# Kernel optimization log

Hardware: AMD Instinct MI355X
Metric: run time of the kernel (lower is better)

Reference implementation:

```python
import jax, jax.numpy as jnp
import numpy as np

SEQ_LEN = 8192
D_K = 128
NEG_BIG = 1000000000.0


def setup_inputs() -> dict:
    key = jax.random.key(0)
    kq, kk, kv = jax.random.split(key, 3)
    q = jax.random.normal(kq, (SEQ_LEN, D_K), dtype=jnp.float32)
    k = jax.random.normal(kk, (SEQ_LEN, D_K), dtype=jnp.float32)
    v = jax.random.normal(kv, (SEQ_LEN, D_K), dtype=jnp.float32)
    return {"q": q, "k": k, "v": v}


def reference(q, k, v):
    # q,k,v: (S, d). Naive attention with causal (look-ahead) mask, masked=True.
    d_k = q.shape[-1]
    scaled_logits = jnp.matmul(q, k.T) / jnp.sqrt(jnp.asarray(d_k, q.dtype))  # (S, S)
    look_ahead_mask = jnp.triu(jnp.ones((SEQ_LEN, SEQ_LEN), dtype=q.dtype), k=1)
    scaled_logits = scaled_logits - look_ahead_mask * NEG_BIG
    attn = jnp.matmul(jax.nn.softmax(scaled_logits, axis=-1), v)  # (S, d)
    return attn
```

## Files before the change

### kernel.cpp

```cpp
#include <hip/hip_runtime.h>
#include <hip/hip_bf16.h>
#include <math.h>

#define S_LEN 8192
#define DK    128
#define BM    128
#define BN    64
#define NQT   (S_LEN / BM)
#define SCALE2 (0.08838834764831845f * 1.4426950408889634f)
#define DEFER_THR 5.0f

typedef __bf16 bf16x8_t __attribute__((ext_vector_type(8)));
typedef __bf16 bf16x4_t __attribute__((ext_vector_type(4)));
typedef __bf16 bf16x2_t __attribute__((ext_vector_type(2)));
typedef float  floatx16 __attribute__((ext_vector_type(16)));
typedef unsigned uintx4 __attribute__((ext_vector_type(4)));
typedef _Float16 half_t;
typedef _Float16 halfx4 __attribute__((ext_vector_type(4)));
typedef _Float16 halfx2 __attribute__((ext_vector_type(2)));

#define GLD16(g, l) __builtin_amdgcn_global_load_lds(                      \
    (const __attribute__((address_space(1))) void*)(g),                    \
    (__attribute__((address_space(3))) void*)(l), 16, 0, 0)

__device__ __forceinline__ float fexp2(float x) {
#if __has_builtin(__builtin_amdgcn_exp2f)
  return __builtin_amdgcn_exp2f(x);
#else
  return exp2f(x);
#endif
}

__device__ __forceinline__ unsigned pack2(float a, float b) {
  bf16x2_t w; w[0] = (__bf16)a; w[1] = (__bf16)b;
  return __builtin_bit_cast(unsigned, w);
}

__device__ __forceinline__ void xswap(unsigned &x, unsigned &y) {
#if __has_builtin(__builtin_amdgcn_permlane32_swap)
  typedef unsigned v2u __attribute__((ext_vector_type(2)));
  v2u t = __builtin_amdgcn_permlane32_swap(x, y, false, false);
  x = t[0]; y = t[1];
#else
  const unsigned sx = (unsigned)__shfl_xor((int)x, 32);
  const unsigned sy = (unsigned)__shfl_xor((int)y, 32);
  const bool lo = ((threadIdx.x & 63) < 32);
  const unsigned nx = lo ? x : sy;
  const unsigned ny = lo ? sx : y;
  x = nx; y = ny;
#endif
}

#define KBLOCKS ((S_LEN * DK) / (256 * 4))
__global__ __launch_bounds__(256) void prep_kv(const float* __restrict__ K,
                                               const float* __restrict__ V,
                                               __bf16* __restrict__ Kb,
                                               __bf16* __restrict__ Vt) {
  const int bx  = blockIdx.x;
  const int tid = threadIdx.x;
  if (bx < KBLOCKS) {
    const int i = (bx * 256 + tid) * 4;
    float4 v = *(const float4*)&K[i];
    bf16x4_t b;
    b[0] = (__bf16)v.x; b[1] = (__bf16)v.y; b[2] = (__bf16)v.z; b[3] = (__bf16)v.w;
    *(bf16x4_t*)&Kb[i] = b;
    return;
  }
  __shared__ __bf16 tl[64][34];
  const int vblk = bx - KBLOCKS;
  const int key0 = (vblk >> 2) * 64;
  const int d0   = (vblk & 3) * 32;
  {
    const int r = tid >> 2, fb = tid & 3;
    const float* vp = V + (size_t)(key0 + r) * DK + d0;
    #pragma unroll
    for (int h = 0; h < 2; ++h) {
      const int f = fb + h * 4;
      float4 v = *(const float4*)(vp + f * 4);
      tl[r][f * 4 + 0] = (__bf16)v.x; tl[r][f * 4 + 1] = (__bf16)v.y;
      tl[r][f * 4 + 2] = (__bf16)v.z; tl[r][f * 4 + 3] = (__bf16)v.w;
    }
  }
  __syncthreads();
  const int d = tid >> 3, kg = tid & 7;
  bf16x8_t b;
  #pragma unroll
  for (int j = 0; j < 8; ++j) b[j] = tl[kg * 8 + j][d];
  *(bf16x8_t*)&Vt[(size_t)(d0 + d) * S_LEN + key0 + kg * 8] = b;
}

__global__ __launch_bounds__(256, 2)
void fa_part(const float* __restrict__ Q, const __bf16* __restrict__ Kb,
             const __bf16* __restrict__ Vtg, float* __restrict__ Out,
             half_t* __restrict__ Opart, float* __restrict__ stats, int C) {
  __shared__ __align__(16) __bf16 Ks[2][BN * DK];
  __shared__ __align__(16) __bf16 Vts[DK * BN];

  const int tid  = threadIdx.x;
  const int wave = tid >> 6;
  const int lane = tid & 63;
  const int l31  = lane & 31;
  const int hh   = lane >> 5;

  const int qtile = (NQT - 1) - blockIdx.x;
  const int g     = blockIdx.y;
  const int nt    = 2 * qtile + 2;
  const int jb0   = g * C;
  if (jb0 >= nt) return;
  const int jb1 = (jb0 + C < nt) ? (jb0 + C) : nt;

  const int h2 = C >> 1;
  const int direct = (qtile < h2);
  const int ca = qtile / h2, cr = qtile - ca * h2;
  const int chunk = h2 * ca * (ca + 1) / 2 + cr * (ca + 1) - h2 + g;

  const int qw  = qtile * BM + wave * 32;
  const int myq = qw + l31;

  bf16x8_t qf[8];
  {
    const float* qrow = Q + (size_t)myq * DK + hh * 8;
    #pragma unroll
    for (int s = 0; s < 8; ++s) {
      float4 x = *(const float4*)(qrow + s * 16);
      float4 y = *(const float4*)(qrow + s * 16 + 4);
      bf16x8_t f;
      f[0]=(__bf16)(x.x*SCALE2); f[1]=(__bf16)(x.y*SCALE2);
      f[2]=(__bf16)(x.z*SCALE2); f[3]=(__bf16)(x.w*SCALE2);
      f[4]=(__bf16)(y.x*SCALE2); f[5]=(__bf16)(y.y*SCALE2);
      f[6]=(__bf16)(y.z*SCALE2); f[7]=(__bf16)(y.w*SCALE2);
      qf[s] = f;
    }
  }

  const __bf16* kp[4]; const __bf16* vp[4]; int loff[4];
  {
    const int ck = (lane & 15) ^ ((wave * 4 + (lane >> 4)) & 15);
    const int cv = (lane & 7) ^ ((lane >> 3) & 7);
    #pragma unroll
    for (int t = 0; t < 4; ++t) {
      const int rk = t * 16 + wave * 4 + (lane >> 4);
      kp[t] = Kb + ((size_t)(jb0 * BN + rk)) * DK + ck * 8;
      const int rv = t * 32 + wave * 8 + (lane >> 3);
      vp[t] = Vtg + (size_t)rv * S_LEN + jb0 * BN + cv * 8;
      loff[t] = t * 2048 + wave * 512;
    }
  }

  floatx16 o_acc[4];
  #pragma unroll
  for (int d = 0; d < 4; ++d)
    #pragma unroll
    for (int r = 0; r < 16; ++r) o_acc[d][r] = 0.f;
  float m_r = -INFINITY, l_r = 0.f;

  #pragma unroll
  for (int t = 0; t < 4; ++t) { GLD16(kp[t], &Ks[0][loff[t]]); kp[t] += BN * DK; }
  __syncthreads();

  int cur = 0;
  for (int jb = jb0; jb < jb1; ++jb) {
    #pragma unroll
    for (int t = 0; t < 4; ++t) { GLD16(vp[t], &Vts[loff[t]]); vp[t] += BN; }
    if (jb + 1 < jb1) {
      #pragma unroll
      for (int t = 0; t < 4; ++t) { GLD16(kp[t], &Ks[cur ^ 1][loff[t]]); kp[t] += BN * DK; }
    }

    const int active = (jb * 64 <= qw + 31);
    floatx16 sv[2];
    unsigned pk[4][4];

    if (active) {
      const __bf16* Kc = Ks[cur];

      bf16x8_t tf[16];
      #pragma unroll
      for (int g1 = 0; g1 < 2; ++g1) {
        const int row = g1 * 32 + l31;
        #pragma unroll
        for (int s = 0; s < 8; ++s)
          tf[g1 * 8 + s] = *(const bf16x8_t*)
              &Kc[row * DK + (((s * 2 + hh) ^ (row & 15)) * 8)];
      }
      __builtin_amdgcn_s_setprio(1);
      #pragma unroll
      for (int g1 = 0; g1 < 2; ++g1) {
        floatx16 acc;
        #pragma unroll
        for (int r = 0; r < 16; ++r) acc[r] = 0.f;
        #pragma unroll
        for (int s = 0; s < 8; ++s)
          acc = __builtin_amdgcn_mfma_f32_32x32x16_bf16(tf[g1 * 8 + s], qf[s],
                                                        acc, 0, 0, 0);
        sv[g1] = acc;
      }
      __builtin_amdgcn_s_setprio(0);

      if (jb * 64 + 63 > qw) {
        #pragma unroll
        for (int g1 = 0; g1 < 2; ++g1)
          #pragma unroll
          for (int r = 0; r < 16; ++r) {
            const int key = jb * 64 + g1 * 32 + (r & 3) + ((r >> 2) << 3) + (hh << 2);
            if (key > myq) sv[g1][r] = -1e30f;
          }
      }

      float pmx[4];
      #pragma unroll
      for (int i = 0; i < 4; ++i)
        pmx[i] = fmaxf(fmaxf(sv[0][i], sv[0][i + 4]),
                       fmaxf(sv[0][i + 8], sv[0][i + 12]));
      #pragma unroll
      for (int i = 0; i < 4; ++i)
        pmx[i] = fmaxf(pmx[i], fmaxf(fmaxf(sv[1][i], sv[1][i + 4]),
                                     fmaxf(sv[1][i + 8], sv[1][i + 12])));
      float pm = fmaxf(fmaxf(pmx[0], pmx[1]), fmaxf(pmx[2], pmx[3]));
      {
        unsigned b0 = __builtin_bit_cast(unsigned, pm), b1 = b0;
        xswap(b0, b1);
        pm = fmaxf(__builtin_bit_cast(float, b0), __builtin_bit_cast(float, b1));
      }

      if (__any(pm > m_r + DEFER_THR)) {
        const float mn = fmaxf(m_r, pm);
        const float al = fexp2(m_r - mn);
        m_r = mn; l_r *= al;
        #pragma unroll
        for (int d = 0; d < 4; ++d)
          #pragma unroll
          for (int r = 0; r < 16; ++r) o_acc[d][r] *= al;
      }

      float rsx[4] = {0.f, 0.f, 0.f, 0.f};
      #pragma unroll
      for (int g1 = 0; g1 < 2; ++g1)
        #pragma unroll
        for (int r = 0; r < 16; ++r) {
          const float pv = fexp2(sv[g1][r] - m_r);
          sv[g1][r] = pv;
          rsx[r & 3] += pv;
        }
      float rs = (rsx[0] + rsx[1]) + (rsx[2] + rsx[3]);
      {
        unsigned b0 = __builtin_bit_cast(unsigned, rs), b1 = b0;
        xswap(b0, b1);
        l_r += __builtin_bit_cast(float, b0) + __builtin_bit_cast(float, b1);
      }

      #pragma unroll
      for (int g1 = 0; g1 < 2; ++g1) {
        unsigned W0 = pack2(sv[g1][0],  sv[g1][1]);
        unsigned W1 = pack2(sv[g1][2],  sv[g1][3]);
        unsigned W2 = pack2(sv[g1][4],  sv[g1][5]);
        unsigned W3 = pack2(sv[g1][6],  sv[g1][7]);
        unsigned W4 = pack2(sv[g1][8],  sv[g1][9]);
        unsigned W5 = pack2(sv[g1][10], sv[g1][11]);
        unsigned W6 = pack2(sv[g1][12], sv[g1][13]);
        unsigned W7 = pack2(sv[g1][14], sv[g1][15]);
        xswap(W0, W2); xswap(W1, W3);
        xswap(W4, W6); xswap(W5, W7);
        pk[g1*2+0][0]=W0; pk[g1*2+0][1]=W1; pk[g1*2+0][2]=W2; pk[g1*2+0][3]=W3;
        pk[g1*2+1][0]=W4; pk[g1*2+1][1]=W5; pk[g1*2+1][2]=W6; pk[g1*2+1][3]=W7;
      }
    }

    __syncthreads();

    if (active) {
      bf16x8_t vf[16];
      #pragma unroll
      for (int ks = 0; ks < 4; ++ks)
        #pragma unroll
        for (int d = 0; d < 4; ++d) {
          const int row = d * 32 + l31;
          vf[ks * 4 + d] = *(const bf16x8_t*)
              &Vts[row * BN + (((ks * 2 + hh) ^ (row & 7)) * 8)];
        }
      __builtin_amdgcn_s_setprio(1);
      #pragma unroll
      for (int ks = 0; ks < 4; ++ks) {
        uintx4 u; u[0]=pk[ks][0]; u[1]=pk[ks][1]; u[2]=pk[ks][2]; u[3]=pk[ks][3];
        const bf16x8_t pf = __builtin_bit_cast(bf16x8_t, u);
        #pragma unroll
        for (int d = 0; d < 4; ++d)
          o_acc[d] = __builtin_amdgcn_mfma_f32_32x32x16_bf16(vf[ks * 4 + d], pf,
                                                             o_acc[d], 0, 0, 0);
      }
      __builtin_amdgcn_s_setprio(0);
    }

    __syncthreads();
    cur ^= 1;
  }

  if (direct) {
    const float inv = (l_r > 0.f) ? (1.0f / l_r) : 0.f;
    float* orow = Out + (size_t)myq * DK;
    #pragma unroll
    for (int d = 0; d < 4; ++d)
      #pragma unroll
      for (int mI = 0; mI < 4; ++mI) {
        float4 st;
        st.x = o_acc[d][mI*4+0] * inv; st.y = o_acc[d][mI*4+1] * inv;
        st.z = o_acc[d][mI*4+2] * inv; st.w = o_acc[d][mI*4+3] * inv;
        *(float4*)&orow[d * 32 + mI * 8 + hh * 4] = st;
      }
  } else {
    const float inv = (l_r > 0.f) ? (1.0f / l_r) : 0.f;
    half_t* orow = Opart + ((size_t)chunk * BM + wave * 32 + l31) * DK;
    #pragma unroll
    for (int d = 0; d < 4; ++d)
      #pragma unroll
      for (int mI = 0; mI < 4; ++mI) {
        halfx4 st;
        st[0] = (half_t)(o_acc[d][mI*4+0] * inv);
        st[1] = (half_t)(o_acc[d][mI*4+1] * inv);
        st[2] = (half_t)(o_acc[d][mI*4+2] * inv);
        st[3] = (half_t)(o_acc[d][mI*4+3] * inv);
        *(halfx4*)&orow[d * 32 + mI * 8 + hh * 4] = st;
      }
    if (hh == 0) {
      stats[((size_t)chunk * BM + wave * 32 + l31) * 2 + 0] = m_r;
      stats[((size_t)chunk * BM + wave * 32 + l31) * 2 + 1] = l_r;
    }
  }
}

__global__ __launch_bounds__(256)
void fa_reduce(const half_t* __restrict__ Opart, const float* __restrict__ stats,
               float* __restrict__ O, int C) {
  const int h2 = C >> 1;
  const int wave = threadIdx.x >> 6, lane = threadIdx.x & 63;
  const int row = h2 * BM + blockIdx.x * 4 + wave;
  const int qt = row >> 7, r = row & 127;

  const int a = qt / h2, rr = qt - a * h2;
  const int base = h2 * a * (a + 1) / 2 + rr * (a + 1) - h2;
  const int nch = (qt + h2) / h2;

  float M = -INFINITY;
  for (int g = 0; g < nch; ++g)
    M = fmaxf(M, stats[((size_t)(base + g) * BM + r) * 2]);

  float L = 0.f, ax = 0.f, ay = 0.f;
  for (int g = 0; g < nch; ++g) {
    const size_t sidx = (size_t)(base + g) * BM + r;
    const float m = stats[sidx * 2];
    const float wl = fexp2(m - M) * stats[sidx * 2 + 1];
    L += wl;
    halfx2 o = *(const halfx2*)&Opart[sidx * DK + lane * 2];
    ax += wl * (float)o[0]; ay += wl * (float)o[1];
  }
  const float inv = 1.f / L;
  float2 res; res.x = ax * inv; res.y = ay * inv;
  *(float2*)&O[(size_t)row * DK + lane * 2] = res;
}

extern "C" void kernel_launch(void* const* d_in, const int* in_sizes, int n_in,
                              void* d_out, int out_size, void* d_ws, size_t ws_size,
                              hipStream_t stream) {
  (void)in_sizes; (void)n_in; (void)out_size;
  const float* q = (const float*)d_in[0];
  const float* k = (const float*)d_in[1];
  const float* v = (const float*)d_in[2];
  float* out = (float*)d_out;

  const size_t conv_bytes = (size_t)S_LEN * DK * 2 * 2;
  const size_t per_chunk  = (size_t)BM * DK * 2 + 2 * BM * 4;

  int C = 2 * NQT; long long nc = 0;
  for (int c = 8; c < 2 * NQT; c += 2) {
    const int hh2 = c / 2;
    const int a = NQT / hh2, rr = NQT - a * hh2;
    const long long F64 = (long long)hh2 * a * (a + 1) / 2 + (long long)rr * (a + 1);
    const long long n = F64 - hh2;
    if (conv_bytes + (size_t)n * per_chunk <= ws_size) { C = c; nc = n; break; }
  }

  __bf16* Kb = (__bf16*)d_ws;
  __bf16* Vt = Kb + (size_t)S_LEN * DK;
  half_t* Opart = (half_t*)(Vt + (size_t)S_LEN * DK);
  float* stats = (float*)(Opart + (size_t)nc * BM * DK);

  prep_kv<<<KBLOCKS + 512, 256, 0, stream>>>(k, v, Kb, Vt);

  const int gy = (2 * NQT + C - 1) / C;
  fa_part<<<dim3(NQT, gy), 256, 0, stream>>>(q, Kb, Vt, out, Opart, stats, C);

  if (nc > 0) {
    const int h2 = C / 2;
    const int nrows = (NQT - h2) * BM;
    fa_reduce<<<nrows / 4, 256, 0, stream>>>(Opart, stats, out, C);
  }
}
```

Before: 124.9 us.

## Double-buffer V tiles and fuse split-K reduction into last-arriving block

```diff
diff --git a/kernel.cpp b/kernel.cpp
--- a/kernel.cpp
+++ b/kernel.cpp
@@ -9,6 +9,7 @@
 #define NQT   (S_LEN / BM)
 #define SCALE2 (0.08838834764831845f * 1.4426950408889634f)
 #define DEFER_THR 5.0f
+#define MAXCH 16
 
 typedef __bf16 bf16x8_t __attribute__((ext_vector_type(8)));
 typedef __bf16 bf16x4_t __attribute__((ext_vector_type(4)));
@@ -17,7 +18,6 @@
 typedef unsigned uintx4 __attribute__((ext_vector_type(4)));
 typedef _Float16 half_t;
 typedef _Float16 halfx4 __attribute__((ext_vector_type(4)));
-typedef _Float16 halfx2 __attribute__((ext_vector_type(2)));
 
 #define GLD16(g, l) __builtin_amdgcn_global_load_lds(                      \
     (const __attribute__((address_space(1))) void*)(g),                    \
@@ -55,9 +55,14 @@
 __global__ __launch_bounds__(256) void prep_kv(const float* __restrict__ K,
                                                const float* __restrict__ V,
                                                __bf16* __restrict__ Kb,
-                                               __bf16* __restrict__ Vt) {
+                                               __bf16* __restrict__ Vt,
+                                               unsigned* __restrict__ counters) {
   const int bx  = blockIdx.x;
   const int tid = threadIdx.x;
+  if (bx >= KBLOCKS + 512) {
+    if (tid < NQT) counters[tid] = 0u;
+    return;
+  }
   if (bx < KBLOCKS) {
     const int i = (bx * 256 + tid) * 4;
     float4 v = *(const float4*)&K[i];
@@ -92,9 +97,11 @@
 __global__ __launch_bounds__(256, 2)
 void fa_part(const float* __restrict__ Q, const __bf16* __restrict__ Kb,
              const __bf16* __restrict__ Vtg, float* __restrict__ Out,
-             half_t* __restrict__ Opart, float* __restrict__ stats, int C) {
+             half_t* __restrict__ Opart, float* __restrict__ stats,
+             unsigned* __restrict__ counters, int C) {
   __shared__ __align__(16) __bf16 Ks[2][BN * DK];
-  __shared__ __align__(16) __bf16 Vts[DK * BN];
+  __shared__ __align__(16) __bf16 Vts[2][DK * BN];
+  __shared__ int lastFlag;
 
   const int tid  = threadIdx.x;
   const int wave = tid >> 6;
@@ -112,7 +119,8 @@
   const int h2 = C >> 1;
   const int direct = (qtile < h2);
   const int ca = qtile / h2, cr = qtile - ca * h2;
-  const int chunk = h2 * ca * (ca + 1) / 2 + cr * (ca + 1) - h2 + g;
+  const int chunkBase = h2 * ca * (ca + 1) / 2 + cr * (ca + 1) - h2;
+  const int chunk = chunkBase + g;
 
   const int qw  = qtile * BM + wave * 32;
   const int myq = qw + l31;
@@ -155,44 +163,47 @@
   float m_r = -INFINITY, l_r = 0.f;
 
   #pragma unroll
-  for (int t = 0; t < 4; ++t) { GLD16(kp[t], &Ks[0][loff[t]]); kp[t] += BN * DK; }
-  __syncthreads();
+  for (int t = 0; t < 4; ++t) GLD16(kp[t], &Ks[0][loff[t]]);
+  #pragma unroll
+  for (int t = 0; t < 4; ++t) GLD16(vp[t], &Vts[0][loff[t]]);
+  if (jb0 + 1 < jb1) {
+    #pragma unroll
+    for (int t = 0; t < 4; ++t) { kp[t] += BN * DK; vp[t] += BN; }
+  }
 
   int cur = 0;
   for (int jb = jb0; jb < jb1; ++jb) {
     #pragma unroll
-    for (int t = 0; t < 4; ++t) { GLD16(vp[t], &Vts[loff[t]]); vp[t] += BN; }
-    if (jb + 1 < jb1) {
-      #pragma unroll
-      for (int t = 0; t < 4; ++t) { GLD16(kp[t], &Ks[cur ^ 1][loff[t]]); kp[t] += BN * DK; }
-    }
-
-    const int active = (jb * 64 <= qw + 31);
-    floatx16 sv[2];
-    unsigned pk[4][4];
-
-    if (active) {
+    for (int t = 0; t < 4; ++t) GLD16(kp[t], &Ks[cur ^ 1][loff[t]]);
+    #pragma unroll
+    for (int t = 0; t < 4; ++t) GLD16(vp[t], &Vts[cur ^ 1][loff[t]]);
+    if (jb + 2 < jb1) {
+      #pragma unroll
+      for (int t = 0; t < 4; ++t) { kp[t] += BN * DK; vp[t] += BN; }
+    }
+
+    asm volatile("s_waitcnt vmcnt(8)" ::: "memory");
+    __builtin_amdgcn_s_barrier();
+    __builtin_amdgcn_sched_barrier(0);
+
+    if (jb * 64 <= qw + 31) {
       const __bf16* Kc = Ks[cur];
-
-      bf16x8_t tf[16];
-      #pragma unroll
-      for (int g1 = 0; g1 < 2; ++g1) {
-        const int row = g1 * 32 + l31;
-        #pragma unroll
-        for (int s = 0; s < 8; ++s)
-          tf[g1 * 8 + s] = *(const bf16x8_t*)
-              &Kc[row * DK + (((s * 2 + hh) ^ (row & 15)) * 8)];
-      }
+      const __bf16* Vc = Vts[cur];
+
+      floatx16 sv[2];
       __builtin_amdgcn_s_setprio(1);
       #pragma unroll
       for (int g1 = 0; g1 < 2; ++g1) {
         floatx16 acc;
         #pragma unroll
         for (int r = 0; r < 16; ++r) acc[r] = 0.f;
-        #pragma unroll
-        for (int s = 0; s < 8; ++s)
-          acc = __builtin_amdgcn_mfma_f32_32x32x16_bf16(tf[g1 * 8 + s], qf[s],
-                                                        acc, 0, 0, 0);
+        const int row = g1 * 32 + l31;
+        #pragma unroll
+        for (int s = 0; s < 8; ++s) {
+          bf16x8_t kf = *(const bf16x8_t*)
+              &Kc[row * DK + (((s * 2 + hh) ^ (row & 15)) * 8)];
+          acc = __builtin_amdgcn_mfma_f32_32x32x16_bf16(kf, qf[s], acc, 0, 0, 0);
+        }
         sv[g1] = acc;
       }
       __builtin_amdgcn_s_setprio(0);
@@ -249,6 +260,7 @@
         l_r += __builtin_bit_cast(float, b0) + __builtin_bit_cast(float, b1);
       }
 
+      unsigned pk[4][4];
       #pragma unroll
       for (int g1 = 0; g1 < 2; ++g1) {
         unsigned W0 = pack2(sv[g1][0],  sv[g1][1]);
@@ -264,34 +276,25 @@
         pk[g1*2+0][0]=W0; pk[g1*2+0][1]=W1; pk[g1*2+0][2]=W2; pk[g1*2+0][3]=W3;
         pk[g1*2+1][0]=W4; pk[g1*2+1][1]=W5; pk[g1*2+1][2]=W6; pk[g1*2+1][3]=W7;
       }
-    }
-
-    __syncthreads();
-
-    if (active) {
-      bf16x8_t vf[16];
-      #pragma unroll
-      for (int ks = 0; ks < 4; ++ks)
-        #pragma unroll
-        for (int d = 0; d < 4; ++d) {
-          const int row = d * 32 + l31;
-          vf[ks * 4 + d] = *(const bf16x8_t*)
-              &Vts[row * BN + (((ks * 2 + hh) ^ (row & 7)) * 8)];
-        }
+
       __builtin_amdgcn_s_setprio(1);
       #pragma unroll
       for (int ks = 0; ks < 4; ++ks) {
         uintx4 u; u[0]=pk[ks][0]; u[1]=pk[ks][1]; u[2]=pk[ks][2]; u[3]=pk[ks][3];
         const bf16x8_t pf = __builtin_bit_cast(bf16x8_t, u);
         #pragma unroll
-        for (int d = 0; d < 4; ++d)
-          o_acc[d] = __builtin_amdgcn_mfma_f32_32x32x16_bf16(vf[ks * 4 + d], pf,
-                                                             o_acc[d], 0, 0, 0);
+        for (int d = 0; d < 4; ++d) {
+          const int row = d * 32 + l31;
+          bf16x8_t vf = *(const bf16x8_t*)
+              &Vc[row * BN + (((ks * 2 + hh) ^ (row & 7)) * 8)];
+          o_acc[d] = __builtin_amdgcn_mfma_f32_32x32x16_bf16(vf, pf, o_acc[d], 0, 0, 0);
+        }
       }
       __builtin_amdgcn_s_setprio(0);
     }
 
-    __syncthreads();
+    __builtin_amdgcn_s_barrier();
+    __builtin_amdgcn_sched_barrier(0);
     cur ^= 1;
   }
 
@@ -307,7 +310,10 @@
         st.z = o_acc[d][mI*4+2] * inv; st.w = o_acc[d][mI*4+3] * inv;
         *(float4*)&orow[d * 32 + mI * 8 + hh * 4] = st;
       }
-  } else {
+    return;
+  }
+
+  {
     const float inv = (l_r > 0.f) ? (1.0f / l_r) : 0.f;
     half_t* orow = Opart + ((size_t)chunk * BM + wave * 32 + l31) * DK;
     #pragma unroll
@@ -326,36 +332,51 @@
       stats[((size_t)chunk * BM + wave * 32 + l31) * 2 + 1] = l_r;
     }
   }
-}
-
-__global__ __launch_bounds__(256)
-void fa_reduce(const half_t* __restrict__ Opart, const float* __restrict__ stats,
-               float* __restrict__ O, int C) {
-  const int h2 = C >> 1;
-  const int wave = threadIdx.x >> 6, lane = threadIdx.x & 63;
-  const int row = h2 * BM + blockIdx.x * 4 + wave;
-  const int qt = row >> 7, r = row & 127;
-
-  const int a = qt / h2, rr = qt - a * h2;
-  const int base = h2 * a * (a + 1) / 2 + rr * (a + 1) - h2;
-  const int nch = (qt + h2) / h2;
-
-  float M = -INFINITY;
-  for (int g = 0; g < nch; ++g)
-    M = fmaxf(M, stats[((size_t)(base + g) * BM + r) * 2]);
-
-  float L = 0.f, ax = 0.f, ay = 0.f;
-  for (int g = 0; g < nch; ++g) {
-    const size_t sidx = (size_t)(base + g) * BM + r;
-    const float m = stats[sidx * 2];
-    const float wl = fexp2(m - M) * stats[sidx * 2 + 1];
-    L += wl;
-    halfx2 o = *(const halfx2*)&Opart[sidx * DK + lane * 2];
-    ax += wl * (float)o[0]; ay += wl * (float)o[1];
-  }
-  const float inv = 1.f / L;
-  float2 res; res.x = ax * inv; res.y = ay * inv;
-  *(float2*)&O[(size_t)row * DK + lane * 2] = res;
+
+  const int nch = (qtile + h2) / h2;
+  __threadfence();
+  __syncthreads();
+  if (tid == 0) {
+    const unsigned old = atomicAdd(&counters[qtile], 1u);
+    lastFlag = (old == (unsigned)(nch - 1)) ? 1 : 0;
+  }
+  __syncthreads();
+  if (!lastFlag) return;
+  __threadfence();
+
+  float* wlf = (float*)Ks;
+  if (tid < BM) {
+    const int r = tid;
+    float M = -INFINITY;
+    for (int g2 = 0; g2 < nch; ++g2)
+      M = fmaxf(M, stats[((size_t)(chunkBase + g2) * BM + r) * 2]);
+    float L = 0.f;
+    for (int g2 = 0; g2 < nch; ++g2) {
+      const size_t sidx = (size_t)(chunkBase + g2) * BM + r;
+      const float wv = fexp2(stats[sidx * 2] - M) * stats[sidx * 2 + 1];
+      wlf[r * (MAXCH + 1) + g2] = wv;
+      L += wv;
+    }
+    const float invL = 1.f / L;
+    for (int g2 = 0; g2 < nch; ++g2) wlf[r * (MAXCH + 1) + g2] *= invL;
+  }
+  __syncthreads();
+
+  #pragma unroll 4
+  for (int i = 0; i < 16; ++i) {
+    const int slot = tid + i * 256;
+    const int r = slot >> 5, c4 = slot & 31;
+    float ax = 0.f, ay = 0.f, az = 0.f, aw = 0.f;
+    for (int g2 = 0; g2 < nch; ++g2) {
+      const float w = wlf[r * (MAXCH + 1) + g2];
+      halfx4 o = *(const halfx4*)
+          &Opart[((size_t)(chunkBase + g2) * BM + r) * DK + c4 * 4];
+      ax += w * (float)o[0]; ay += w * (float)o[1];
+      az += w * (float)o[2]; aw += w * (float)o[3];
+    }
+    float4 res; res.x = ax; res.y = ay; res.z = az; res.w = aw;
+    *(float4*)&Out[((size_t)(qtile * BM + r)) * DK + c4 * 4] = res;
+  }
 }
 
 extern "C" void kernel_launch(void* const* d_in, const int* in_sizes, int n_in,
@@ -376,22 +397,18 @@
     const int a = NQT / hh2, rr = NQT - a * hh2;
     const long long F64 = (long long)hh2 * a * (a + 1) / 2 + (long long)rr * (a + 1);
     const long long n = F64 - hh2;
-    if (conv_bytes + (size_t)n * per_chunk <= ws_size) { C = c; nc = n; break; }
+    if (conv_bytes + (size_t)n * per_chunk + NQT * 4 <= ws_size) { C = c; nc = n; break; }
   }
 
   __bf16* Kb = (__bf16*)d_ws;
   __bf16* Vt = Kb + (size_t)S_LEN * DK;
   half_t* Opart = (half_t*)(Vt + (size_t)S_LEN * DK);
   float* stats = (float*)(Opart + (size_t)nc * BM * DK);
-
-  prep_kv<<<KBLOCKS + 512, 256, 0, stream>>>(k, v, Kb, Vt);
+  unsigned* counters = (unsigned*)(stats + (size_t)nc * BM * 2);
+
+  prep_kv<<<KBLOCKS + 513, 256, 0, stream>>>(k, v, Kb, Vt, counters);
 
   const int gy = (2 * NQT + C - 1) / C;
-  fa_part<<<dim3(NQT, gy), 256, 0, stream>>>(q, Kb, Vt, out, Opart, stats, C);
-
-  if (nc > 0) {
-    const int h2 = C / 2;
-    const int nrows = (NQT - h2) * BM;
-    fa_reduce<<<nrows / 4, 256, 0, stream>>>(Opart, stats, out, C);
-  }
-}
+  fa_part<<<dim3(NQT, gy), 256, 0, stream>>>(q, Kb, Vt, out, Opart, stats,
+                                             counters, C);
+}
```

New measurement: 226.9 us. 81.7% more time.

## Load K and V tiles directly from global into registers, dropping LDS staging

Applied to the files above, without the earlier changes.

```diff
diff --git a/kernel.cpp b/kernel.cpp
--- a/kernel.cpp
+++ b/kernel.cpp
@@ -18,10 +18,6 @@
 typedef _Float16 half_t;
 typedef _Float16 halfx4 __attribute__((ext_vector_type(4)));
 typedef _Float16 halfx2 __attribute__((ext_vector_type(2)));
-
-#define GLD16(g, l) __builtin_amdgcn_global_load_lds(                      \
-    (const __attribute__((address_space(1))) void*)(g),                    \
-    (__attribute__((address_space(3))) void*)(l), 16, 0, 0)
 
 __device__ __forceinline__ float fexp2(float x) {
 #if __has_builtin(__builtin_amdgcn_exp2f)
@@ -89,13 +85,10 @@
   *(bf16x8_t*)&Vt[(size_t)(d0 + d) * S_LEN + key0 + kg * 8] = b;
 }
 
-__global__ __launch_bounds__(256, 2)
+__global__ __launch_bounds__(256, 3)
 void fa_part(const float* __restrict__ Q, const __bf16* __restrict__ Kb,
              const __bf16* __restrict__ Vtg, float* __restrict__ Out,
              half_t* __restrict__ Opart, float* __restrict__ stats, int C) {
-  __shared__ __align__(16) __bf16 Ks[2][BN * DK];
-  __shared__ __align__(16) __bf16 Vts[DK * BN];
-
   const int tid  = threadIdx.x;
   const int wave = tid >> 6;
   const int lane = tid & 63;
@@ -116,6 +109,9 @@
 
   const int qw  = qtile * BM + wave * 32;
   const int myq = qw + l31;
+
+  const int jbw1_ = qtile * 2 + (wave >> 1) + 1;
+  const int jbw1 = (jb1 < jbw1_) ? jb1 : jbw1_;
 
   bf16x8_t qf[8];
   {
@@ -133,19 +129,14 @@
     }
   }
 
-  const __bf16* kp[4]; const __bf16* vp[4]; int loff[4];
-  {
-    const int ck = (lane & 15) ^ ((wave * 4 + (lane >> 4)) & 15);
-    const int cv = (lane & 7) ^ ((lane >> 3) & 7);
-    #pragma unroll
-    for (int t = 0; t < 4; ++t) {
-      const int rk = t * 16 + wave * 4 + (lane >> 4);
-      kp[t] = Kb + ((size_t)(jb0 * BN + rk)) * DK + ck * 8;
-      const int rv = t * 32 + wave * 8 + (lane >> 3);
-      vp[t] = Vtg + (size_t)rv * S_LEN + jb0 * BN + cv * 8;
-      loff[t] = t * 2048 + wave * 512;
-    }
-  }
+  const __bf16* kp[2];
+  const __bf16* vp[4];
+  #pragma unroll
+  for (int g1 = 0; g1 < 2; ++g1)
+    kp[g1] = Kb + ((size_t)(jb0 * BN + g1 * 32 + l31)) * DK + hh * 8;
+  #pragma unroll
+  for (int d = 0; d < 4; ++d)
+    vp[d] = Vtg + (size_t)(d * 32 + l31) * S_LEN + jb0 * BN + hh * 8;
 
   floatx16 o_acc[4];
   #pragma unroll
@@ -154,145 +145,121 @@
     for (int r = 0; r < 16; ++r) o_acc[d][r] = 0.f;
   float m_r = -INFINITY, l_r = 0.f;
 
-  #pragma unroll
-  for (int t = 0; t < 4; ++t) { GLD16(kp[t], &Ks[0][loff[t]]); kp[t] += BN * DK; }
-  __syncthreads();
-
-  int cur = 0;
-  for (int jb = jb0; jb < jb1; ++jb) {
-    #pragma unroll
-    for (int t = 0; t < 4; ++t) { GLD16(vp[t], &Vts[loff[t]]); vp[t] += BN; }
-    if (jb + 1 < jb1) {
-      #pragma unroll
-      for (int t = 0; t < 4; ++t) { GLD16(kp[t], &Ks[cur ^ 1][loff[t]]); kp[t] += BN * DK; }
-    }
-
-    const int active = (jb * 64 <= qw + 31);
+  for (int jb = jb0; jb < jbw1; ++jb) {
+    bf16x8_t kf[16];
+    #pragma unroll
+    for (int g1 = 0; g1 < 2; ++g1)
+      #pragma unroll
+      for (int s = 0; s < 8; ++s)
+        kf[g1 * 8 + s] = *(const bf16x8_t*)(kp[g1] + s * 16);
+
     floatx16 sv[2];
-    unsigned pk[4][4];
-
-    if (active) {
-      const __bf16* Kc = Ks[cur];
-
-      bf16x8_t tf[16];
-      #pragma unroll
-      for (int g1 = 0; g1 < 2; ++g1) {
-        const int row = g1 * 32 + l31;
-        #pragma unroll
-        for (int s = 0; s < 8; ++s)
-          tf[g1 * 8 + s] = *(const bf16x8_t*)
-              &Kc[row * DK + (((s * 2 + hh) ^ (row & 15)) * 8)];
-      }
-      __builtin_amdgcn_s_setprio(1);
-      #pragma unroll
-      for (int g1 = 0; g1 < 2; ++g1) {
-        floatx16 acc;
-        #pragma unroll
-        for (int r = 0; r < 16; ++r) acc[r] = 0.f;
-        #pragma unroll
-        for (int s = 0; s < 8; ++s)
-          acc = __builtin_amdgcn_mfma_f32_32x32x16_bf16(tf[g1 * 8 + s], qf[s],
-                                                        acc, 0, 0, 0);
-        sv[g1] = acc;
-      }
-      __builtin_amdgcn_s_setprio(0);
-
-      if (jb * 64 + 63 > qw) {
-        #pragma unroll
-        for (int g1 = 0; g1 < 2; ++g1)
-          #pragma unroll
-          for (int r = 0; r < 16; ++r) {
-            const int key = jb * 64 + g1 * 32 + (r & 3) + ((r >> 2) << 3) + (hh << 2);
-            if (key > myq) sv[g1][r] = -1e30f;
-          }
-      }
-
-      float pmx[4];
-      #pragma unroll
-      for (int i = 0; i < 4; ++i)
-        pmx[i] = fmaxf(fmaxf(sv[0][i], sv[0][i + 4]),
-                       fmaxf(sv[0][i + 8], sv[0][i + 12]));
-      #pragma unroll
-      for (int i = 0; i < 4; ++i)
-        pmx[i] = fmaxf(pmx[i], fmaxf(fmaxf(sv[1][i], sv[1][i + 4]),
-                                     fmaxf(sv[1][i + 8], sv[1][i + 12])));
-      float pm = fmaxf(fmaxf(pmx[0], pmx[1]), fmaxf(pmx[2], pmx[3]));
-      {
-        unsigned b0 = __builtin_bit_cast(unsigned, pm), b1 = b0;
-        xswap(b0, b1);
-        pm = fmaxf(__builtin_bit_cast(float, b0), __builtin_bit_cast(float, b1));
-      }
-
-      if (__any(pm > m_r + DEFER_THR)) {
-        const float mn = fmaxf(m_r, pm);
-        const float al = fexp2(m_r - mn);
-        m_r = mn; l_r *= al;
-        #pragma unroll
-        for (int d = 0; d < 4; ++d)
-          #pragma unroll
-          for (int r = 0; r < 16; ++r) o_acc[d][r] *= al;
-      }
-
-      float rsx[4] = {0.f, 0.f, 0.f, 0.f};
+    __builtin_amdgcn_s_setprio(1);
+    #pragma unroll
+    for (int g1 = 0; g1 < 2; ++g1) {
+      floatx16 acc;
+      #pragma unroll
+      for (int r = 0; r < 16; ++r) acc[r] = 0.f;
+      #pragma unroll
+      for (int s = 0; s < 8; ++s)
+        acc = __builtin_amdgcn_mfma_f32_32x32x16_bf16(kf[g1 * 8 + s], qf[s],
+                                                      acc, 0, 0, 0);
+      sv[g1] = acc;
+    }
+    __builtin_amdgcn_s_setprio(0);
+
+    bf16x8_t vf[16];
+    #pragma unroll
+    for (int ks = 0; ks < 4; ++ks)
+      #pragma unroll
+      for (int d = 0; d < 4; ++d)
+        vf[ks * 4 + d] = *(const bf16x8_t*)(vp[d] + ks * 16);
+
+    if (jb * 64 + 63 > qw) {
       #pragma unroll
       for (int g1 = 0; g1 < 2; ++g1)
         #pragma unroll
         for (int r = 0; r < 16; ++r) {
-          const float pv = fexp2(sv[g1][r] - m_r);
-          sv[g1][r] = pv;
-          rsx[r & 3] += pv;
+          const int key = jb * 64 + g1 * 32 + (r & 3) + ((r >> 2) << 3) + (hh << 2);
+          if (key > myq) sv[g1][r] = -1e30f;
         }
-      float rs = (rsx[0] + rsx[1]) + (rsx[2] + rsx[3]);
-      {
-        unsigned b0 = __builtin_bit_cast(unsigned, rs), b1 = b0;
-        xswap(b0, b1);
-        l_r += __builtin_bit_cast(float, b0) + __builtin_bit_cast(float, b1);
+    }
+
+    float pmx[4];
+    #pragma unroll
+    for (int i = 0; i < 4; ++i)
+      pmx[i] = fmaxf(fmaxf(sv[0][i], sv[0][i + 4]),
+                     fmaxf(sv[0][i + 8], sv[0][i + 12]));
+    #pragma unroll
+    for (int i = 0; i < 4; ++i)
+      pmx[i] = fmaxf(pmx[i], fmaxf(fmaxf(sv[1][i], sv[1][i + 4]),
+                                   fmaxf(sv[1][i + 8], sv[1][i + 12])));
+    float pm = fmaxf(fmaxf(pmx[0], pmx[1]), fmaxf(pmx[2], pmx[3]));
+    {
+      unsigned b0 = __builtin_bit_cast(unsigned, pm), b1 = b0;
+      xswap(b0, b1);
+      pm = fmaxf(__builtin_bit_cast(float, b0), __builtin_bit_cast(float, b1));
+    }
+
+    if (__any(pm > m_r + DEFER_THR)) {
+      const float mn = fmaxf(m_r, pm);
+      const float al = fexp2(m_r - mn);
+      m_r = mn; l_r *= al;
+      #pragma unroll
+      for (int d = 0; d < 4; ++d)
+        #pragma unroll
+        for (int r = 0; r < 16; ++r) o_acc[d][r] *= al;
+    }
+
+    float rsx[4] = {0.f, 0.f, 0.f, 0.f};
+    #pragma unroll
+    for (int g1 = 0; g1 < 2; ++g1)
+      #pragma unroll
+      for (int r = 0; r < 16; ++r) {
+        const float pv = fexp2(sv[g1][r] - m_r);
+        sv[g1][r] = pv;
+        rsx[r & 3] += pv;
       }
-
-      #pragma unroll
-      for (int g1 = 0; g1 < 2; ++g1) {
-        unsigned W0 = pack2(sv[g1][0],  sv[g1][1]);
-        unsigned W1 = pack2(sv[g1][2],  sv[g1][3]);
-        unsigned W2 = pack2(sv[g1][4],  sv[g1][5]);
-        unsigned W3 = pack2(sv[g1][6],  sv[g1][7]);
-        unsigned W4 = pack2(sv[g1][8],  sv[g1][9]);
-        unsigned W5 = pack2(sv[g1][10], sv[g1][11]);
-        unsigned W6 = pack2(sv[g1][12], sv[g1][13]);
-        unsigned W7 = pack2(sv[g1][14], sv[g1][15]);
-        xswap(W0, W2); xswap(W1, W3);
-        xswap(W4, W6); xswap(W5, W7);
-        pk[g1*2+0][0]=W0; pk[g1*2+0][1]=W1; pk[g1*2+0][2]=W2; pk[g1*2+0][3]=W3;
-        pk[g1*2+1][0]=W4; pk[g1*2+1][1]=W5; pk[g1*2+1][2]=W6; pk[g1*2+1][3]=W7;
-      }
-    }
-
-    __syncthreads();
-
-    if (active) {
-      bf16x8_t vf[16];
-      #pragma unroll
-      for (int ks = 0; ks < 4; ++ks)
-        #pragma unroll
-        for (int d = 0; d < 4; ++d) {
-          const int row = d * 32 + l31;
-          vf[ks * 4 + d] = *(const bf16x8_t*)
-              &Vts[row * BN + (((ks * 2 + hh) ^ (row & 7)) * 8)];
-        }
-      __builtin_amdgcn_s_setprio(1);
-      #pragma unroll
-      for (int ks = 0; ks < 4; ++ks) {
-        uintx4 u; u[0]=pk[ks][0]; u[1]=pk[ks][1]; u[2]=pk[ks][2]; u[3]=pk[ks][3];
-        const bf16x8_t pf = __builtin_bit_cast(bf16x8_t, u);
-        #pragma unroll
-        for (int d = 0; d < 4; ++d)
-          o_acc[d] = __builtin_amdgcn_mfma_f32_32x32x16_bf16(vf[ks * 4 + d], pf,
-                                                             o_acc[d], 0, 0, 0);
-      }
-      __builtin_amdgcn_s_setprio(0);
-    }
-
-    __syncthreads();
-    cur ^= 1;
+    float rs = (rsx[0] + rsx[1]) + (rsx[2] + rsx[3]);
+    {
+      unsigned b0 = __builtin_bit_cast(unsigned, rs), b1 = b0;
+      xswap(b0, b1);
+      l_r += __builtin_bit_cast(float, b0) + __builtin_bit_cast(float, b1);
+    }
+
+    unsigned pk[4][4];
+    #pragma unroll
+    for (int g1 = 0; g1 < 2; ++g1) {
+      unsigned W0 = pack2(sv[g1][0],  sv[g1][1]);
+      unsigned W1 = pack2(sv[g1][2],  sv[g1][3]);
+      unsigned W2 = pack2(sv[g1][4],  sv[g1][5]);
+      unsigned W3 = pack2(sv[g1][6],  sv[g1][7]);
+      unsigned W4 = pack2(sv[g1][8],  sv[g1][9]);
+      unsigned W5 = pack2(sv[g1][10], sv[g1][11]);
+      unsigned W6 = pack2(sv[g1][12], sv[g1][13]);
+      unsigned W7 = pack2(sv[g1][14], sv[g1][15]);
+      xswap(W0, W2); xswap(W1, W3);
+      xswap(W4, W6); xswap(W5, W7);
+      pk[g1*2+0][0]=W0; pk[g1*2+0][1]=W1; pk[g1*2+0][2]=W2; pk[g1*2+0][3]=W3;
+      pk[g1*2+1][0]=W4; pk[g1*2+1][1]=W5; pk[g1*2+1][2]=W6; pk[g1*2+1][3]=W7;
+    }
+
+    __builtin_amdgcn_s_setprio(1);
+    #pragma unroll
+    for (int ks = 0; ks < 4; ++ks) {
+      uintx4 u; u[0]=pk[ks][0]; u[1]=pk[ks][1]; u[2]=pk[ks][2]; u[3]=pk[ks][3];
+      const bf16x8_t pf = __builtin_bit_cast(bf16x8_t, u);
+      #pragma unroll
+      for (int d = 0; d < 4; ++d)
+        o_acc[d] = __builtin_amdgcn_mfma_f32_32x32x16_bf16(vf[ks * 4 + d], pf,
+                                                           o_acc[d], 0, 0, 0);
+    }
+    __builtin_amdgcn_s_setprio(0);
+
+    #pragma unroll
+    for (int g1 = 0; g1 < 2; ++g1) kp[g1] += BN * DK;
+    #pragma unroll
+    for (int d = 0; d < 4; ++d) vp[d] += BN;
   }
 
   if (direct) {
```

After: 241.8 us. 1.94x slower.
